# Performance work log

Hardware: AMD Instinct MI355X
Metric: run time of the kernel (lower is better)

The kernel has to match this reference:

```python
import jax, jax.numpy as jnp
import numpy as np

N_NODES = 50000
N_EDGES = 800000
IN_DIM, HID, OUT = 64, 128, 32
BN_EPS = 1e-5


def setup_inputs() -> dict:
    key = jax.random.key(0)
    ks = jax.random.split(key, 24)
    def w(k, shape, fan_in):
        return jax.random.normal(k, shape, dtype=jnp.float32) * (1.0 / np.sqrt(fan_in))
    inp = {
        "x": jax.random.normal(ks[0], (N_NODES, IN_DIM), dtype=jnp.float32),
        "edge_index": jax.random.randint(ks[1], (2, N_EDGES), 0, N_NODES, dtype=jnp.int64),
        # layer 0 GIN MLP: in -> hid -> hid
        "w1_0": w(ks[2], (IN_DIM, HID), IN_DIM), "b1_0": jnp.zeros((HID,), jnp.float32),
        "w2_0": w(ks[3], (HID, HID), HID),       "b2_0": jnp.zeros((HID,), jnp.float32),
        # skip projection for layer 0 (in_dim != hidden_dim -> Linear)
        "skip_w": w(ks[4], (IN_DIM, HID), IN_DIM), "skip_b": jnp.zeros((HID,), jnp.float32),
        # batchnorm params (layers 0 and 1 only)
        "bn_g0": jnp.ones((HID,), jnp.float32), "bn_b0": jnp.zeros((HID,), jnp.float32),
        # layer 1 GIN MLP: hid -> hid -> hid
        "w1_1": w(ks[5], (HID, HID), HID), "b1_1": jnp.zeros((HID,), jnp.float32),
        "w2_1": w(ks[6], (HID, HID), HID), "b2_1": jnp.zeros((HID,), jnp.float32),
        "bn_g1": jnp.ones((HID,), jnp.float32), "bn_b1": jnp.zeros((HID,), jnp.float32),
        # layer 2 GIN MLP: hid -> hid -> out
        "w1_2": w(ks[7], (HID, HID), HID), "b1_2": jnp.zeros((HID,), jnp.float32),
        "w2_2": w(ks[8], (HID, OUT), HID), "b2_2": jnp.zeros((OUT,), jnp.float32),
    }
    return inp


def _gin_conv(h, src, dst, n, W1, b1, W2, b2):
    # GINConv (eps=0): mlp((1+eps)*x_i + sum_{j in N(i)} x_j)
    agg = jax.ops.segment_sum(h[src], dst, num_segments=n)  # [N, d]
    z = h + agg
    return jax.nn.relu(z @ W1 + b1) @ W2 + b2


def _bn(h, g, b):
    # training-mode batchnorm over nodes (batch statistics, biased var)
    m = h.mean(0)
    v = jnp.mean((h - m) ** 2, axis=0)
    return g * (h - m) * jax.lax.rsqrt(v + BN_EPS) + b


def reference(x, edge_index, w1_0, b1_0, w2_0, b2_0, skip_w, skip_b, bn_g0, bn_b0,
              w1_1, b1_1, w2_1, b2_1, bn_g1, bn_b1, w1_2, b1_2, w2_2, b2_2):
    src, dst = edge_index[0], edge_index[1]
    n = x.shape[0]
    # layer 0: conv -> bn -> +skip_proj(residual) -> relu (dropout = identity in eval)
    h = _gin_conv(x, src, dst, n, w1_0, b1_0, w2_0, b2_0)
    h = _bn(h, bn_g0, bn_b0)
    h = h + (x @ skip_w + skip_b)
    residual = h
    h = jax.nn.relu(h)
    # layer 1: conv -> bn -> +residual (Identity skip) -> relu
    h = _gin_conv(h, src, dst, n, w1_1, b1_1, w2_1, b2_1)
    h = _bn(h, bn_g1, bn_b1)
    h = h + residual
    h = jax.nn.relu(h)
    # layer 2: conv only (no bn since i >= len(bns), no skip/relu since i == num_layers-1)
    h = _gin_conv(h, src, dst, n, w1_2, b1_2, w2_2, b2_2)
    return h
```

## Files before the change

kernel.cpp:

```cpp
#include <hip/hip_runtime.h>
#include <hip/hip_bf16.h>


#define HID 128
#define NPART 8
#define ABLK 256
#define BBLK 128
#define CAP 64

typedef __attribute__((ext_vector_type(8))) __bf16 bf16x8;
typedef __attribute__((ext_vector_type(4))) float f32x4;

__device__ __forceinline__ ushort f2b(float f) {
    uint u = __builtin_bit_cast(uint, f);
    u = (u + 0x7fffu + ((u >> 16) & 1u)) >> 16;
    return (ushort)u;
}
__device__ __forceinline__ float b2f(ushort s) {
    return __builtin_bit_cast(float, (uint)s << 16);
}
__device__ __forceinline__ float lo16(uint u) { return __builtin_bit_cast(float, u << 16); }
__device__ __forceinline__ float hi16(uint u) { return __builtin_bit_cast(float, u & 0xffff0000u); }
__device__ __forceinline__ uint packbf(float a, float b) {
    return (uint)f2b(a) | ((uint)f2b(b) << 16);
}

__launch_bounds__(256)
__global__ void ecount_kernel(const int* __restrict__ ei, int* __restrict__ bc,
                              int E, int pchunk) {
    __shared__ int cnt[NPART];
    if (threadIdx.x < NPART) cnt[threadIdx.x] = 0;
    __syncthreads();
    const int epb = (E + ABLK - 1) / ABLK;
    const int e0 = blockIdx.x * epb, e1 = min(e0 + epb, E);
    for (int e = e0 + threadIdx.x; e < e1; e += 256) {
        int d = ei[E + e];
        atomicAdd(&cnt[d / pchunk], 1);
    }
    __syncthreads();
    if (threadIdx.x < NPART) bc[threadIdx.x * ABLK + blockIdx.x] = cnt[threadIdx.x];
}

__launch_bounds__(1024)
__global__ void escan_kernel(int* __restrict__ bc) {
    __shared__ int ls[1024];
    const int t = threadIdx.x;
    const int v0 = bc[2 * t], v1 = bc[2 * t + 1];
    ls[t] = v0 + v1;
    __syncthreads();
    for (int off = 1; off < 1024; off <<= 1) {
        int tmp = (t >= off) ? ls[t - off] : 0;
        __syncthreads();
        ls[t] += tmp;
        __syncthreads();
    }
    const int excl = ls[t] - (v0 + v1);
    bc[2 * t] = excl;
    bc[2 * t + 1] = excl + v0;
}

__launch_bounds__(256)
__global__ void edist_kernel(const int* __restrict__ ei, const int* __restrict__ bc,
                             int2* __restrict__ ebuf, int E, int pchunk) {
    __shared__ int base[NPART];
    if (threadIdx.x < NPART) base[threadIdx.x] = bc[threadIdx.x * ABLK + blockIdx.x];
    __syncthreads();
    const int epb = (E + ABLK - 1) / ABLK;
    const int e0 = blockIdx.x * epb, e1 = min(e0 + epb, E);
    for (int e = e0 + threadIdx.x; e < e1; e += 256) {
        int s = ei[e], d = ei[E + e];
        int pos = atomicAdd(&base[d / pchunk], 1);
        ebuf[pos] = make_int2(s, d);
    }
}

__launch_bounds__(256)
__global__ void scatterf_kernel(const int2* __restrict__ ebuf, const int* __restrict__ bc,
                                int* __restrict__ deg, int* __restrict__ csr, int E) {
    const int part = blockIdx.x & (NPART - 1);
    const int blk  = blockIdx.x >> 3;
    const int pstart = bc[part * ABLK];
    const int pend = (part == NPART - 1) ? E : bc[(part + 1) * ABLK];
    const int epb = (pend - pstart + BBLK - 1) / BBLK;
    const int e0 = pstart + blk * epb, e1 = min(e0 + epb, pend);
    for (int e = e0 + threadIdx.x; e < e1; e += 256) {
        int2 ed = ebuf[e];
        int slot = atomicAdd(&deg[ed.y], 1);
        if (slot < CAP) csr[((size_t)ed.y << 6) + slot] = ed.x;
    }
}

__launch_bounds__(256)
__global__ void padfill_kernel(const int* __restrict__ deg, int* __restrict__ csr,
                               int* __restrict__ rowlen, int n) {
    const int nd = blockIdx.x * 256 + threadIdx.x;
    if (nd >= n) return;
    const int d = min(deg[nd], CAP);
    const int pd = min((d + 7) & ~7, CAP);
    for (int q = d; q < pd; q++) csr[((size_t)nd << 6) + q] = n;
    rowlen[nd] = pd;
}

struct PrepAll {
    const float* src[7];
    ushort* dst[7];
    int K[7];
    int N[7];
    int off[8];
};

__launch_bounds__(256)
__global__ void wprep_kernel(PrepAll a) {
    const int b = blockIdx.x;
    int m = 0;
    while (m < 6 && b >= a.off[m + 1]) m++;
    const int K = a.K[m], N = a.N[m];
    const int e = (b - a.off[m]) * 256 + threadIdx.x;
    if (e >= K * N) return;
    const int n = e / K, k = e % K;
    a.dst[m][e] = f2b(a.src[m][(size_t)k * N + n]);
}

__global__ void x2bf_kernel(const float* __restrict__ x, ushort* __restrict__ xb,
                            float* __restrict__ bn0, float* __restrict__ bn1,
                            int* __restrict__ deg, uint* __restrict__ xb_sent,
                            uint* __restrict__ agg_sent, int n, int total4) {
    const int gi = blockIdx.x * 256 + threadIdx.x;
    if (gi < 2048) { bn0[gi] = 0.f; bn1[gi] = 0.f; }
    if (blockIdx.x == 0) {
        if (threadIdx.x < 64) agg_sent[threadIdx.x] = 0;
        else if (threadIdx.x < 96) xb_sent[threadIdx.x - 64] = 0;
    }
    if (gi < n) deg[gi] = 0;
    if (gi < total4) {
        float4 v = reinterpret_cast<const float4*>(x)[gi];
        ushort4 o;
        o.x = f2b(v.x); o.y = f2b(v.y); o.z = f2b(v.z); o.w = f2b(v.w);
        reinterpret_cast<ushort4*>(xb)[gi] = o;
    }
}

template <int K1, int NC2, bool SKIP, bool OUTBF, bool STATS>
__launch_bounds__(512)
__global__ void fused_layer(const ushort* __restrict__ table,
                            const int* __restrict__ rowlen, const int* __restrict__ csr,
                            const ushort* __restrict__ W1t, const float* __restrict__ b1,
                            const ushort* __restrict__ W2t, const float* __restrict__ b2,
                            float* __restrict__ convf, ushort* __restrict__ convb,
                            const ushort* __restrict__ skw, const float* __restrict__ skb,
                            float* __restrict__ skipout, float* __restrict__ bnsums,
                            int M) {
    __shared__ ushort Zt[64 * K1];
    __shared__ ushort Yt[64 * 128];
    __shared__ float bnloc[STATS ? 256 : 1];
    const int tid = threadIdx.x;
    const int w = tid >> 6, lane = tid & 63;
    const int rb0 = blockIdx.x * 64;
    constexpr int ZROWB = K1 * 2;

    if (STATS && tid < 256) bnloc[tid] = 0.f;

    if constexpr (K1 == 128) {
        const uint* t2 = reinterpret_cast<const uint*>(table);
#pragma unroll
        for (int i = 0; i < 8; i++) {
            const int rt = w * 8 + i;
            const int nd = min(rb0 + rt, M - 1);
            const int s = nd << 6;
            const int e = s + rowlen[nd];
            uint v = t2[(size_t)nd * 64 + lane];
            float ax = lo16(v), ay = hi16(v);
            for (int k = s; k < e; k += 8) {
#pragma unroll
                for (int j = 0; j < 8; j++) {
                    uint u = t2[(size_t)csr[k + j] * 64 + lane];
                    ax += lo16(u);
                    ay += hi16(u);
                }
            }
            *reinterpret_cast<uint*>(reinterpret_cast<char*>(Zt) +
                (((uint)(rt * 256 + lane * 4)) ^ ((rt & 7) << 4))) = packbf(ax, ay);
        }
    } else {
        const uint* t2 = reinterpret_cast<const uint*>(table);
        const int half = lane >> 5, li = lane & 31;
#pragma unroll
        for (int i = 0; i < 4; i++) {
            const int rt = w * 8 + i * 2 + half;
            const int nd = min(rb0 + rt, M - 1);
            const int s = nd << 6;
            const int e = s + rowlen[nd];
            uint v = t2[(size_t)nd * 32 + li];
            float ax = lo16(v), ay = hi16(v);
            for (int k = s; k < e; k += 8) {
#pragma unroll
                for (int j = 0; j < 8; j++) {
                    uint u = t2[(size_t)csr[k + j] * 32 + li];
                    ax += lo16(u);
                    ay += hi16(u);
                }
            }
            *reinterpret_cast<uint*>(reinterpret_cast<char*>(Zt) +
                (((uint)(rt * 128 + li * 4)) ^ ((rt & 7) << 4))) = packbf(ax, ay);
        }
    }
    __syncthreads();

    const int wr = w >> 2, wc = w & 3;
    const int lr = lane & 15, hg = lane >> 4;
    const int xorv = (lr & 7) << 4;

    {
        f32x4 a00 = {}, a01 = {}, a10 = {}, a11 = {};
#pragma unroll
        for (int k0 = 0; k0 < K1; k0 += 32) {
            const uint o0 = (uint)((wr * 32 + lr) * ZROWB + k0 * 2 + hg * 16) ^ xorv;
            const uint o1 = (uint)((wr * 32 + 16 + lr) * ZROWB + k0 * 2 + hg * 16) ^ xorv;
            bf16x8 za0 = *reinterpret_cast<const bf16x8*>(reinterpret_cast<const char*>(Zt) + o0);
            bf16x8 za1 = *reinterpret_cast<const bf16x8*>(reinterpret_cast<const char*>(Zt) + o1);
            bf16x8 wb0 = *reinterpret_cast<const bf16x8*>(W1t + (size_t)(wc * 32 + lr) * K1 + k0 + hg * 8);
            bf16x8 wb1 = *reinterpret_cast<const bf16x8*>(W1t + (size_t)(wc * 32 + 16 + lr) * K1 + k0 + hg * 8);
            a00 = __builtin_amdgcn_mfma_f32_16x16x32_bf16(za0, wb0, a00, 0, 0, 0);
            a01 = __builtin_amdgcn_mfma_f32_16x16x32_bf16(za0, wb1, a01, 0, 0, 0);
            a10 = __builtin_amdgcn_mfma_f32_16x16x32_bf16(za1, wb0, a10, 0, 0, 0);
            a11 = __builtin_amdgcn_mfma_f32_16x16x32_bf16(za1, wb1, a11, 0, 0, 0);
        }
        const int c0 = wc * 32 + lr, c1 = wc * 32 + 16 + lr;
        const float bv0 = b1[c0], bv1 = b1[c1];
        f32x4 accs[2][2] = {{a00, a01}, {a10, a11}};
#pragma unroll
        for (int m = 0; m < 2; m++) {
#pragma unroll
            for (int j = 0; j < 4; j++) {
                const int row = wr * 32 + m * 16 + hg * 4 + j;
                const uint sw = (uint)((row & 7) << 4);
                *reinterpret_cast<ushort*>(reinterpret_cast<char*>(Yt) + ((uint)(row * 256 + c0 * 2) ^ sw)) =
                    f2b(fmaxf(accs[m][0][j] + bv0, 0.f));
                *reinterpret_cast<ushort*>(reinterpret_cast<char*>(Yt) + ((uint)(row * 256 + c1 * 2) ^ sw)) =
                    f2b(fmaxf(accs[m][1][j] + bv1, 0.f));
            }
        }
    }
    __syncthreads();

    if constexpr (SKIP) {
        const uint* x2 = reinterpret_cast<const uint*>(table);
#pragma unroll
        for (int pp = 0; pp < 4; pp++) {
            const int rt = pp * 16 + (tid >> 5);
            const int cu = tid & 31;
            const int nd = min(rb0 + rt, M - 1);
            uint v = x2[(size_t)nd * 32 + cu];
            const uint boff = (uint)(rt * 128 + cu * 4) ^ ((rt & 7) << 4);
            *reinterpret_cast<uint*>(reinterpret_cast<char*>(Zt) + boff) = v;
        }
    }

    if (NC2 == 128 || w < 2) {
        const int wr2 = (NC2 == 128) ? wr : w;
        const int cb2 = (NC2 == 128) ? wc * 32 : 0;
        f32x4 d00 = {}, d01 = {}, d10 = {}, d11 = {};
#pragma unroll
        for (int k0 = 0; k0 < 128; k0 += 32) {
            const uint o0 = (uint)((wr2 * 32 + lr) * 256 + k0 * 2 + hg * 16) ^ xorv;
            const uint o1 = (uint)((wr2 * 32 + 16 + lr) * 256 + k0 * 2 + hg * 16) ^ xorv;
            bf16x8 ya0 = *reinterpret_cast<const bf16x8*>(reinterpret_cast<const char*>(Yt) + o0);
            bf16x8 ya1 = *reinterpret_cast<const bf16x8*>(reinterpret_cast<const char*>(Yt) + o1);
            bf16x8 wb0 = *reinterpret_cast<const bf16x8*>(W2t + (size_t)(cb2 + lr) * 128 + k0 + hg * 8);
            bf16x8 wb1 = *reinterpret_cast<const bf16x8*>(W2t + (size_t)(cb2 + 16 + lr) * 128 + k0 + hg * 8);
            d00 = __builtin_amdgcn_mfma_f32_16x16x32_bf16(ya0, wb0, d00, 0, 0, 0);
            d01 = __builtin_amdgcn_mfma_f32_16x16x32_bf16(ya0, wb1, d01, 0, 0, 0);
            d10 = __builtin_amdgcn_mfma_f32_16x16x32_bf16(ya1, wb0, d10, 0, 0, 0);
            d11 = __builtin_amdgcn_mfma_f32_16x16x32_bf16(ya1, wb1, d11, 0, 0, 0);
        }
        const int c0 = cb2 + lr, c1 = cb2 + 16 + lr;
        const float bv0 = b2[c0], bv1 = b2[c1];
        f32x4 accs[2][2] = {{d00, d01}, {d10, d11}};
        float s0 = 0.f, q0 = 0.f, s1 = 0.f, q1 = 0.f;
#pragma unroll
        for (int m = 0; m < 2; m++) {
#pragma unroll
            for (int j = 0; j < 4; j++) {
                const int row = rb0 + wr2 * 32 + m * 16 + hg * 4 + j;
                if (row < M) {
                    const float v0 = accs[m][0][j] + bv0;
                    const float v1 = accs[m][1][j] + bv1;
                    if (STATS) {
                        s0 += v0; q0 += v0 * v0;
                        s1 += v1; q1 += v1 * v1;
                    }
                    if constexpr (OUTBF) {
                        convb[(size_t)row * NC2 + c0] = f2b(v0);
                        convb[(size_t)row * NC2 + c1] = f2b(v1);
                    } else {
                        convf[(size_t)row * NC2 + c0] = v0;
                        convf[(size_t)row * NC2 + c1] = v1;
                    }
                }
            }
        }
        if (STATS) {
            atomicAdd(&bnloc[c0], s0);
            atomicAdd(&bnloc[c1], s1);
            atomicAdd(&bnloc[128 + c0], q0);
            atomicAdd(&bnloc[128 + c1], q1);
        }
    }

    if constexpr (SKIP) {
        __syncthreads();
        f32x4 s00 = {}, s01 = {}, s10 = {}, s11 = {};
#pragma unroll
        for (int k0 = 0; k0 < 64; k0 += 32) {
            const uint o0 = (uint)((wr * 32 + lr) * 128 + k0 * 2 + hg * 16) ^ xorv;
            const uint o1 = (uint)((wr * 32 + 16 + lr) * 128 + k0 * 2 + hg * 16) ^ xorv;
            bf16x8 za0 = *reinterpret_cast<const bf16x8*>(reinterpret_cast<const char*>(Zt) + o0);
            bf16x8 za1 = *reinterpret_cast<const bf16x8*>(reinterpret_cast<const char*>(Zt) + o1);
            bf16x8 wb0 = *reinterpret_cast<const bf16x8*>(skw + (size_t)(wc * 32 + lr) * 64 + k0 + hg * 8);
            bf16x8 wb1 = *reinterpret_cast<const bf16x8*>(skw + (size_t)(wc * 32 + 16 + lr) * 64 + k0 + hg * 8);
            s00 = __builtin_amdgcn_mfma_f32_16x16x32_bf16(za0, wb0, s00, 0, 0, 0);
            s01 = __builtin_amdgcn_mfma_f32_16x16x32_bf16(za0, wb1, s01, 0, 0, 0);
            s10 = __builtin_amdgcn_mfma_f32_16x16x32_bf16(za1, wb0, s10, 0, 0, 0);
            s11 = __builtin_amdgcn_mfma_f32_16x16x32_bf16(za1, wb1, s11, 0, 0, 0);
        }
        const int c0 = wc * 32 + lr, c1 = wc * 32 + 16 + lr;
        const float bv0 = skb[c0], bv1 = skb[c1];
        f32x4 accs[2][2] = {{s00, s01}, {s10, s11}};
#pragma unroll
        for (int m = 0; m < 2; m++) {
#pragma unroll
            for (int j = 0; j < 4; j++) {
                const int row = rb0 + wr * 32 + m * 16 + hg * 4 + j;
                if (row < M) {
                    skipout[(size_t)row * 128 + c0] = accs[m][0][j] + bv0;
                    skipout[(size_t)row * 128 + c1] = accs[m][1][j] + bv1;
                }
            }
        }
    }

    if constexpr (STATS) {
        __syncthreads();
        if (tid < 256) atomicAdd(&bnsums[((blockIdx.x & 7) << 8) + tid], bnloc[tid]);
    }
}

template <bool WRITE_RES>
__global__ void bn_apply_kernel(const ushort* __restrict__ conv, const float* __restrict__ sums,
                                const float* __restrict__ gamma, const float* __restrict__ beta,
                                const float* __restrict__ add, float* __restrict__ resf,
                                ushort* __restrict__ outb, int total2, int n) {
    int i = blockIdx.x * blockDim.x + threadIdx.x;
    if (i >= total2) return;
    const int c0 = (i & 63) * 2, c1 = c0 + 1;
    float S0 = 0.f, S1 = 0.f, Q0 = 0.f, Q1 = 0.f;
#pragma unroll
    for (int b = 0; b < 8; b++) {
        const float* bp = sums + (b << 8);
        S0 += bp[c0]; S1 += bp[c1];
        Q0 += bp[128 + c0]; Q1 += bp[128 + c1];
    }
    const float inv = 1.f / (float)n;
    const float m0 = S0 * inv, m1 = S1 * inv;
    const float v0 = Q0 * inv - m0 * m0;
    const float v1 = Q1 * inv - m1 * m1;
    const float sc0 = gamma[c0] * rsqrtf(v0 + 1e-5f);
    const float sc1 = gamma[c1] * rsqrtf(v1 + 1e-5f);
    const uint u = reinterpret_cast<const uint*>(conv)[i];
    const float2 ad = reinterpret_cast<const float2*>(add)[i];
    const float val0 = (lo16(u) - m0) * sc0 + beta[c0] + ad.x;
    const float val1 = (hi16(u) - m1) * sc1 + beta[c1] + ad.y;
    if (WRITE_RES) reinterpret_cast<float2*>(resf)[i] = make_float2(val0, val1);
    reinterpret_cast<uint*>(outb)[i] = packbf(fmaxf(val0, 0.f), fmaxf(val1, 0.f));
}

extern "C" void kernel_launch(void* const* d_in, const int* in_sizes, int n_in,
                              void* d_out, int out_size, void* d_ws, size_t ws_size,
                              hipStream_t stream) {
    const float* x      = (const float*)d_in[0];
    const int*   ei     = (const int*)d_in[1];
    const float* w1_0   = (const float*)d_in[2];
    const float* b1_0   = (const float*)d_in[3];
    const float* w2_0   = (const float*)d_in[4];
    const float* b2_0   = (const float*)d_in[5];
    const float* skip_w = (const float*)d_in[6];
    const float* skip_b = (const float*)d_in[7];
    const float* bn_g0  = (const float*)d_in[8];
    const float* bn_b0  = (const float*)d_in[9];
    const float* w1_1   = (const float*)d_in[10];
    const float* b1_1   = (const float*)d_in[11];
    const float* w2_1   = (const float*)d_in[12];
    const float* b2_1   = (const float*)d_in[13];
    const float* bn_g1  = (const float*)d_in[14];
    const float* bn_b1  = (const float*)d_in[15];
    const float* w1_2   = (const float*)d_in[16];
    const float* b1_2   = (const float*)d_in[17];
    const float* w2_2   = (const float*)d_in[18];
    const float* b2_2   = (const float*)d_in[19];

    const int N = in_sizes[0] / 64;
    const int E = in_sizes[1] / 2;
    const int pchunk = (N + NPART - 1) / NPART;

    char* p = (char*)d_ws;
    auto carve = [&](size_t bytes) -> void* {
        void* q = (void*)p;
        p += (bytes + 255) & ~(size_t)255;
        return q;
    };
    int*   deg    = (int*)carve((size_t)N * 4);
    int*   rowlen = (int*)carve((size_t)N * 4);
    int*   csr    = (int*)carve((size_t)N * CAP * 4);
    int*   bc     = (int*)carve((size_t)NPART * ABLK * 4);
    int2*  ebuf   = (int2*)carve((size_t)E * 8);
    float* bnsums0 = (float*)carve(2048 * 4);
    float* bnsums1 = (float*)carve(2048 * 4);
    ushort* w1_0t = (ushort*)carve(64 * 128 * 2);
    ushort* w2_0t = (ushort*)carve(128 * 128 * 2);
    ushort* skwt  = (ushort*)carve(64 * 128 * 2);
    ushort* w1_1t = (ushort*)carve(128 * 128 * 2);
    ushort* w2_1t = (ushort*)carve(128 * 128 * 2);
    ushort* w1_2t = (ushort*)carve(128 * 128 * 2);
    ushort* w2_2t = (ushort*)carve(128 * 32 * 2);
    ushort* x_bf  = (ushort*)carve((size_t)(N + 1) * 64 * 2);
    ushort* aggin = (ushort*)carve((size_t)(N + 1) * HID * 2);
    ushort* convB = (ushort*)carve((size_t)N * HID * 2);
    float* bufC_f = (float*)carve((size_t)N * HID * 4);

    const int NB  = (N + 255) / 256;
    const int EWB2 = (N * 64 + 255) / 256;
    const int FUSE_G = (N + 63) / 64;

    PrepAll pa;
    pa.src[0] = w1_0; pa.dst[0] = w1_0t; pa.K[0] = 64;  pa.N[0] = 128;
    pa.src[1] = w2_0; pa.dst[1] = w2_0t; pa.K[1] = 128; pa.N[1] = 128;
    pa.src[2] = skip_w; pa.dst[2] = skwt; pa.K[2] = 64; pa.N[2] = 128;
    pa.src[3] = w1_1; pa.dst[3] = w1_1t; pa.K[3] = 128; pa.N[3] = 128;
    pa.src[4] = w2_1; pa.dst[4] = w2_1t; pa.K[4] = 128; pa.N[4] = 128;
    pa.src[5] = w1_2; pa.dst[5] = w1_2t; pa.K[5] = 128; pa.N[5] = 128;
    pa.src[6] = w2_2; pa.dst[6] = w2_2t; pa.K[6] = 128; pa.N[6] = 32;
    int off = 0;
    for (int m = 0; m < 7; m++) { pa.off[m] = off; off += (pa.K[m] * pa.N[m]) / 256; }
    pa.off[7] = off;
    wprep_kernel<<<off, 256, 0, stream>>>(pa);
    x2bf_kernel<<<(N * 64 / 4 + 255) / 256, 256, 0, stream>>>(
        x, x_bf, bnsums0, bnsums1, deg,
        reinterpret_cast<uint*>(x_bf + (size_t)N * 64),
        reinterpret_cast<uint*>(aggin + (size_t)N * HID), N, N * 64 / 4);

    ecount_kernel<<<ABLK, 256, 0, stream>>>(ei, bc, E, pchunk);
    escan_kernel<<<1, 1024, 0, stream>>>(bc);
    edist_kernel<<<ABLK, 256, 0, stream>>>(ei, bc, ebuf, E, pchunk);
    scatterf_kernel<<<NPART * BBLK, 256, 0, stream>>>(ebuf, bc, deg, csr, E);
    padfill_kernel<<<NB, 256, 0, stream>>>(deg, csr, rowlen, N);

    fused_layer<64, 128, true, true, true><<<FUSE_G, 512, 0, stream>>>(
        x_bf, rowlen, csr, w1_0t, b1_0, w2_0t, b2_0, nullptr, convB, skwt, skip_b, bufC_f, bnsums0, N);
    bn_apply_kernel<true><<<EWB2, 256, 0, stream>>>(convB, bnsums0, bn_g0, bn_b0, bufC_f, bufC_f, aggin, N * 64, N);

    fused_layer<128, 128, false, true, true><<<FUSE_G, 512, 0, stream>>>(
        aggin, rowlen, csr, w1_1t, b1_1, w2_1t, b2_1, nullptr, convB, nullptr, nullptr, nullptr, bnsums1, N);
    bn_apply_kernel<false><<<EWB2, 256, 0, stream>>>(convB, bnsums1, bn_g1, bn_b1, bufC_f, nullptr, aggin, N * 64, N);

    fused_layer<128, 32, false, false, false><<<FUSE_G, 512, 0, stream>>>(
        aggin, rowlen, csr, w1_2t, b1_2, w2_2t, b2_2, (float*)d_out, nullptr, nullptr, nullptr, nullptr, nullptr, N);
}
```

Baseline: 266.9 us.

## Split aggregation into XCD-sliced gather kernel and separate MFMA MLP kernel

After: 394.7 us. 1.48x slower.

```diff
diff --git a/kernel.cpp b/kernel.cpp
--- a/kernel.cpp
+++ b/kernel.cpp
@@ -15,9 +15,6 @@
     uint u = __builtin_bit_cast(uint, f);
     u = (u + 0x7fffu + ((u >> 16) & 1u)) >> 16;
     return (ushort)u;
-}
-__device__ __forceinline__ float b2f(ushort s) {
-    return __builtin_bit_cast(float, (uint)s << 16);
 }
 __device__ __forceinline__ float lo16(uint u) { return __builtin_bit_cast(float, u << 16); }
 __device__ __forceinline__ float hi16(uint u) { return __builtin_bit_cast(float, u & 0xffff0000u); }
@@ -76,7 +73,7 @@
 
 __launch_bounds__(256)
 __global__ void scatterf_kernel(const int2* __restrict__ ebuf, const int* __restrict__ bc,
-                                int* __restrict__ deg, int* __restrict__ csr, int E) {
+                                int* __restrict__ deg, ushort* __restrict__ csr, int E) {
     const int part = blockIdx.x & (NPART - 1);
     const int blk  = blockIdx.x >> 3;
     const int pstart = bc[part * ABLK];
@@ -86,18 +83,18 @@
     for (int e = e0 + threadIdx.x; e < e1; e += 256) {
         int2 ed = ebuf[e];
         int slot = atomicAdd(&deg[ed.y], 1);
-        if (slot < CAP) csr[((size_t)ed.y << 6) + slot] = ed.x;
-    }
-}
-
-__launch_bounds__(256)
-__global__ void padfill_kernel(const int* __restrict__ deg, int* __restrict__ csr,
+        if (slot < CAP) csr[((size_t)ed.y << 6) + slot] = (ushort)ed.x;
+    }
+}
+
+__launch_bounds__(256)
+__global__ void padfill_kernel(const int* __restrict__ deg, ushort* __restrict__ csr,
                                int* __restrict__ rowlen, int n) {
     const int nd = blockIdx.x * 256 + threadIdx.x;
     if (nd >= n) return;
     const int d = min(deg[nd], CAP);
     const int pd = min((d + 7) & ~7, CAP);
-    for (int q = d; q < pd; q++) csr[((size_t)nd << 6) + q] = n;
+    for (int q = d; q < pd; q++) csr[((size_t)nd << 6) + q] = (ushort)n;
     rowlen[nd] = pd;
 }
 
@@ -140,99 +137,86 @@
     }
 }
 
+template <int RU, int NSLICE>
+__launch_bounds__(256)
+__global__ void agg_slice2(const ushort* __restrict__ table, const int* __restrict__ rowlen,
+                           const ushort* __restrict__ csr, ushort* __restrict__ z, int n) {
+    constexpr int NPARTN = 8 / NSLICE;
+    const int p8 = blockIdx.x & 7;
+    const int slice = p8 % NSLICE;
+    const int part = p8 / NSLICE;
+    const int cb = blockIdx.x >> 3;
+    const int npp = (n + NPARTN - 1) / NPARTN;
+    const int n0 = part * npp;
+    const int n1 = min(n0 + npp, n);
+    const int w = threadIdx.x >> 6, lane = threadIdx.x & 63;
+    const int li = lane & 15, qi = lane >> 4;
+    const int col = slice * 16 + li;
+    const uint* t2 = reinterpret_cast<const uint*>(table);
+    uint* z2 = reinterpret_cast<uint*>(z);
+    const int base = n0 + (cb * 4 + w) * 16;
+    for (int i = 0; i < 16; i++) {
+        const int nd = base + i;
+        if (nd >= n1) break;
+        const int s = nd << 6;
+        const int len = rowlen[nd];
+        uint sv = (qi == 0) ? t2[(size_t)nd * RU + col] : 0u;
+        float ax = lo16(sv), ay = hi16(sv);
+        for (int k = qi; k < len; k += 8) {
+            const int i0 = csr[s + k];
+            const int i1 = csr[s + k + 4];
+            const uint u0 = t2[(size_t)i0 * RU + col];
+            const uint u1 = t2[(size_t)i1 * RU + col];
+            ax += lo16(u0); ay += hi16(u0);
+            ax += lo16(u1); ay += hi16(u1);
+        }
+        ax += __shfl_xor(ax, 16); ay += __shfl_xor(ay, 16);
+        ax += __shfl_xor(ax, 32); ay += __shfl_xor(ay, 32);
+        if (qi == 0) z2[(size_t)nd * RU + col] = packbf(ax, ay);
+    }
+}
+
 template <int K1, int NC2, bool SKIP, bool OUTBF, bool STATS>
-__launch_bounds__(512)
-__global__ void fused_layer(const ushort* __restrict__ table,
-                            const int* __restrict__ rowlen, const int* __restrict__ csr,
-                            const ushort* __restrict__ W1t, const float* __restrict__ b1,
-                            const ushort* __restrict__ W2t, const float* __restrict__ b2,
-                            float* __restrict__ convf, ushort* __restrict__ convb,
-                            const ushort* __restrict__ skw, const float* __restrict__ skb,
-                            float* __restrict__ skipout, float* __restrict__ bnsums,
-                            int M) {
-    __shared__ ushort Zt[64 * K1];
-    __shared__ ushort Yt[64 * 128];
+__launch_bounds__(256)
+__global__ void mlp_layer(const ushort* __restrict__ Z,
+                          const ushort* __restrict__ W1t, const float* __restrict__ b1,
+                          const ushort* __restrict__ W2t, const float* __restrict__ b2,
+                          float* __restrict__ convf, ushort* __restrict__ convb,
+                          const ushort* __restrict__ skw, const float* __restrict__ skb,
+                          float* __restrict__ skipout, const ushort* __restrict__ xbf,
+                          float* __restrict__ bnsums, int M) {
+    __shared__ ushort Yt[32 * 128];
     __shared__ float bnloc[STATS ? 256 : 1];
     const int tid = threadIdx.x;
     const int w = tid >> 6, lane = tid & 63;
-    const int rb0 = blockIdx.x * 64;
-    constexpr int ZROWB = K1 * 2;
-
-    if (STATS && tid < 256) bnloc[tid] = 0.f;
-
-    if constexpr (K1 == 128) {
-        const uint* t2 = reinterpret_cast<const uint*>(table);
-#pragma unroll
-        for (int i = 0; i < 8; i++) {
-            const int rt = w * 8 + i;
-            const int nd = min(rb0 + rt, M - 1);
-            const int s = nd << 6;
-            const int e = s + rowlen[nd];
-            uint v = t2[(size_t)nd * 64 + lane];
-            float ax = lo16(v), ay = hi16(v);
-            for (int k = s; k < e; k += 8) {
-#pragma unroll
-                for (int j = 0; j < 8; j++) {
-                    uint u = t2[(size_t)csr[k + j] * 64 + lane];
-                    ax += lo16(u);
-                    ay += hi16(u);
-                }
-            }
-            *reinterpret_cast<uint*>(reinterpret_cast<char*>(Zt) +
-                (((uint)(rt * 256 + lane * 4)) ^ ((rt & 7) << 4))) = packbf(ax, ay);
-        }
-    } else {
-        const uint* t2 = reinterpret_cast<const uint*>(table);
-        const int half = lane >> 5, li = lane & 31;
-#pragma unroll
-        for (int i = 0; i < 4; i++) {
-            const int rt = w * 8 + i * 2 + half;
-            const int nd = min(rb0 + rt, M - 1);
-            const int s = nd << 6;
-            const int e = s + rowlen[nd];
-            uint v = t2[(size_t)nd * 32 + li];
-            float ax = lo16(v), ay = hi16(v);
-            for (int k = s; k < e; k += 8) {
-#pragma unroll
-                for (int j = 0; j < 8; j++) {
-                    uint u = t2[(size_t)csr[k + j] * 32 + li];
-                    ax += lo16(u);
-                    ay += hi16(u);
-                }
-            }
-            *reinterpret_cast<uint*>(reinterpret_cast<char*>(Zt) +
-                (((uint)(rt * 128 + li * 4)) ^ ((rt & 7) << 4))) = packbf(ax, ay);
-        }
-    }
-    __syncthreads();
-
-    const int wr = w >> 2, wc = w & 3;
+    const int rb0 = blockIdx.x * 32;
     const int lr = lane & 15, hg = lane >> 4;
     const int xorv = (lr & 7) << 4;
+    const int r0 = min(rb0 + lr, M - 1), r1 = min(rb0 + 16 + lr, M - 1);
+
+    if (STATS && tid < 256) bnloc[tid] = 0.f;
 
     {
         f32x4 a00 = {}, a01 = {}, a10 = {}, a11 = {};
 #pragma unroll
         for (int k0 = 0; k0 < K1; k0 += 32) {
-            const uint o0 = (uint)((wr * 32 + lr) * ZROWB + k0 * 2 + hg * 16) ^ xorv;
-            const uint o1 = (uint)((wr * 32 + 16 + lr) * ZROWB + k0 * 2 + hg * 16) ^ xorv;
-            bf16x8 za0 = *reinterpret_cast<const bf16x8*>(reinterpret_cast<const char*>(Zt) + o0);
-            bf16x8 za1 = *reinterpret_cast<const bf16x8*>(reinterpret_cast<const char*>(Zt) + o1);
-            bf16x8 wb0 = *reinterpret_cast<const bf16x8*>(W1t + (size_t)(wc * 32 + lr) * K1 + k0 + hg * 8);
-            bf16x8 wb1 = *reinterpret_cast<const bf16x8*>(W1t + (size_t)(wc * 32 + 16 + lr) * K1 + k0 + hg * 8);
+            bf16x8 za0 = *reinterpret_cast<const bf16x8*>(Z + (size_t)r0 * K1 + k0 + hg * 8);
+            bf16x8 za1 = *reinterpret_cast<const bf16x8*>(Z + (size_t)r1 * K1 + k0 + hg * 8);
+            bf16x8 wb0 = *reinterpret_cast<const bf16x8*>(W1t + (size_t)(w * 32 + lr) * K1 + k0 + hg * 8);
+            bf16x8 wb1 = *reinterpret_cast<const bf16x8*>(W1t + (size_t)(w * 32 + 16 + lr) * K1 + k0 + hg * 8);
             a00 = __builtin_amdgcn_mfma_f32_16x16x32_bf16(za0, wb0, a00, 0, 0, 0);
             a01 = __builtin_amdgcn_mfma_f32_16x16x32_bf16(za0, wb1, a01, 0, 0, 0);
             a10 = __builtin_amdgcn_mfma_f32_16x16x32_bf16(za1, wb0, a10, 0, 0, 0);
             a11 = __builtin_amdgcn_mfma_f32_16x16x32_bf16(za1, wb1, a11, 0, 0, 0);
         }
-        const int c0 = wc * 32 + lr, c1 = wc * 32 + 16 + lr;
+        const int c0 = w * 32 + lr, c1 = w * 32 + 16 + lr;
         const float bv0 = b1[c0], bv1 = b1[c1];
         f32x4 accs[2][2] = {{a00, a01}, {a10, a11}};
 #pragma unroll
         for (int m = 0; m < 2; m++) {
 #pragma unroll
             for (int j = 0; j < 4; j++) {
-                const int row = wr * 32 + m * 16 + hg * 4 + j;
+                const int row = m * 16 + hg * 4 + j;
                 const uint sw = (uint)((row & 7) << 4);
                 *reinterpret_cast<ushort*>(reinterpret_cast<char*>(Yt) + ((uint)(row * 256 + c0 * 2) ^ sw)) =
                     f2b(fmaxf(accs[m][0][j] + bv0, 0.f));
@@ -241,29 +225,44 @@
             }
         }
     }
+
+    if constexpr (SKIP) {
+        f32x4 s00 = {}, s01 = {}, s10 = {}, s11 = {};
+#pragma unroll
+        for (int k0 = 0; k0 < 64; k0 += 32) {
+            bf16x8 za0 = *reinterpret_cast<const bf16x8*>(xbf + (size_t)r0 * 64 + k0 + hg * 8);
+            bf16x8 za1 = *reinterpret_cast<const bf16x8*>(xbf + (size_t)r1 * 64 + k0 + hg * 8);
+            bf16x8 wb0 = *reinterpret_cast<const bf16x8*>(skw + (size_t)(w * 32 + lr) * 64 + k0 + hg * 8);
+            bf16x8 wb1 = *reinterpret_cast<const bf16x8*>(skw + (size_t)(w * 32 + 16 + lr) * 64 + k0 + hg * 8);
+            s00 = __builtin_amdgcn_mfma_f32_16x16x32_bf16(za0, wb0, s00, 0, 0, 0);
+            s01 = __builtin_amdgcn_mfma_f32_16x16x32_bf16(za0, wb1, s01, 0, 0, 0);
+            s10 = __builtin_amdgcn_mfma_f32_16x16x32_bf16(za1, wb0, s10, 0, 0, 0);
+            s11 = __builtin_amdgcn_mfma_f32_16x16x32_bf16(za1, wb1, s11, 0, 0, 0);
+        }
+        const int c0 = w * 32 + lr, c1 = w * 32 + 16 + lr;
+        const float bv0 = skb[c0], bv1 = skb[c1];
+        f32x4 accs[2][2] = {{s00, s01}, {s10, s11}};
+#pragma unroll
+        for (int m = 0; m < 2; m++) {
+#pragma unroll
+            for (int j = 0; j < 4; j++) {
+                const int row = rb0 + m * 16 + hg * 4 + j;
+                if (row < M) {
+                    skipout[(size_t)row * 128 + c0] = accs[m][0][j] + bv0;
+                    skipout[(size_t)row * 128 + c1] = accs[m][1][j] + bv1;
+                }
+            }
+        }
+    }
     __syncthreads();
 
-    if constexpr (SKIP) {
-        const uint* x2 = reinterpret_cast<const uint*>(table);
-#pragma unroll
-        for (int pp = 0; pp < 4; pp++) {
-            const int rt = pp * 16 + (tid >> 5);
-            const int cu = tid & 31;
-            const int nd = min(rb0 + rt, M - 1);
-            uint v = x2[(size_t)nd * 32 + cu];
-            const uint boff = (uint)(rt * 128 + cu * 4) ^ ((rt & 7) << 4);
-            *reinterpret_cast<uint*>(reinterpret_cast<char*>(Zt) + boff) = v;
-        }
-    }
-
-    if (NC2 == 128 || w < 2) {
-        const int wr2 = (NC2 == 128) ? wr : w;
-        const int cb2 = (NC2 == 128) ? wc * 32 : 0;
+    if (NC2 == 128 || w == 0) {
+        const int cb2 = (NC2 == 128) ? w * 32 : 0;
         f32x4 d00 = {}, d01 = {}, d10 = {}, d11 = {};
 #pragma unroll
         for (int k0 = 0; k0 < 128; k0 += 32) {
-            const uint o0 = (uint)((wr2 * 32 + lr) * 256 + k0 * 2 + hg * 16) ^ xorv;
-            const uint o1 = (uint)((wr2 * 32 + 16 + lr) * 256 + k0 * 2 + hg * 16) ^ xorv;
+            const uint o0 = (uint)(lr * 256 + k0 * 2 + hg * 16) ^ xorv;
+            const uint o1 = (uint)((16 + lr) * 256 + k0 * 2 + hg * 16) ^ xorv;
             bf16x8 ya0 = *reinterpret_cast<const bf16x8*>(reinterpret_cast<const char*>(Yt) + o0);
             bf16x8 ya1 = *reinterpret_cast<const bf16x8*>(reinterpret_cast<const char*>(Yt) + o1);
             bf16x8 wb0 = *reinterpret_cast<const bf16x8*>(W2t + (size_t)(cb2 + lr) * 128 + k0 + hg * 8);
@@ -281,7 +280,7 @@
         for (int m = 0; m < 2; m++) {
 #pragma unroll
             for (int j = 0; j < 4; j++) {
-                const int row = rb0 + wr2 * 32 + m * 16 + hg * 4 + j;
+                const int row = rb0 + m * 16 + hg * 4 + j;
                 if (row < M) {
                     const float v0 = accs[m][0][j] + bv0;
                     const float v1 = accs[m][1][j] + bv1;
@@ -304,38 +303,6 @@
             atomicAdd(&bnloc[c1], s1);
             atomicAdd(&bnloc[128 + c0], q0);
             atomicAdd(&bnloc[128 + c1], q1);
-        }
-    }
-
-    if constexpr (SKIP) {
-        __syncthreads();
-        f32x4 s00 = {}, s01 = {}, s10 = {}, s11 = {};
-#pragma unroll
-        for (int k0 = 0; k0 < 64; k0 += 32) {
-            const uint o0 = (uint)((wr * 32 + lr) * 128 + k0 * 2 + hg * 16) ^ xorv;
-            const uint o1 = (uint)((wr * 32 + 16 + lr) * 128 + k0 * 2 + hg * 16) ^ xorv;
-            bf16x8 za0 = *reinterpret_cast<const bf16x8*>(reinterpret_cast<const char*>(Zt) + o0);
-            bf16x8 za1 = *reinterpret_cast<const bf16x8*>(reinterpret_cast<const char*>(Zt) + o1);
-            bf16x8 wb0 = *reinterpret_cast<const bf16x8*>(skw + (size_t)(wc * 32 + lr) * 64 + k0 + hg * 8);
-            bf16x8 wb1 = *reinterpret_cast<const bf16x8*>(skw + (size_t)(wc * 32 + 16 + lr) * 64 + k0 + hg * 8);
-            s00 = __builtin_amdgcn_mfma_f32_16x16x32_bf16(za0, wb0, s00, 0, 0, 0);
-            s01 = __builtin_amdgcn_mfma_f32_16x16x32_bf16(za0, wb1, s01, 0, 0, 0);
-            s10 = __builtin_amdgcn_mfma_f32_16x16x32_bf16(za1, wb0, s10, 0, 0, 0);
-            s11 = __builtin_amdgcn_mfma_f32_16x16x32_bf16(za1, wb1, s11, 0, 0, 0);
-        }
-        const int c0 = wc * 32 + lr, c1 = wc * 32 + 16 + lr;
-        const float bv0 = skb[c0], bv1 = skb[c1];
-        f32x4 accs[2][2] = {{s00, s01}, {s10, s11}};
-#pragma unroll
-        for (int m = 0; m < 2; m++) {
-#pragma unroll
-            for (int j = 0; j < 4; j++) {
-                const int row = rb0 + wr * 32 + m * 16 + hg * 4 + j;
-                if (row < M) {
-                    skipout[(size_t)row * 128 + c0] = accs[m][0][j] + bv0;
-                    skipout[(size_t)row * 128 + c1] = accs[m][1][j] + bv1;
-                }
-            }
         }
     }
 
@@ -408,11 +375,11 @@
         p += (bytes + 255) & ~(size_t)255;
         return q;
     };
-    int*   deg    = (int*)carve((size_t)N * 4);
-    int*   rowlen = (int*)carve((size_t)N * 4);
-    int*   csr    = (int*)carve((size_t)N * CAP * 4);
-    int*   bc     = (int*)carve((size_t)NPART * ABLK * 4);
-    int2*  ebuf   = (int2*)carve((size_t)E * 8);
+    int*    deg    = (int*)carve((size_t)N * 4);
+    int*    rowlen = (int*)carve((size_t)N * 4);
+    ushort* csr    = (ushort*)carve((size_t)N * CAP * 2);
+    int*    bc     = (int*)carve((size_t)NPART * ABLK * 4);
+    int2*   ebuf   = (int2*)carve((size_t)E * 8);
     float* bnsums0 = (float*)carve(2048 * 4);
     float* bnsums1 = (float*)carve(2048 * 4);
     ushort* w1_0t = (ushort*)carve(64 * 128 * 2);
@@ -424,12 +391,17 @@
     ushort* w2_2t = (ushort*)carve(128 * 32 * 2);
     ushort* x_bf  = (ushort*)carve((size_t)(N + 1) * 64 * 2);
     ushort* aggin = (ushort*)carve((size_t)(N + 1) * HID * 2);
+    ushort* bufZ  = (ushort*)carve((size_t)N * HID * 2);
     ushort* convB = (ushort*)carve((size_t)N * HID * 2);
     float* bufC_f = (float*)carve((size_t)N * HID * 4);
 
     const int NB  = (N + 255) / 256;
     const int EWB2 = (N * 64 + 255) / 256;
-    const int FUSE_G = (N + 63) / 64;
+    const int MLP_G = (N + 31) / 32;
+    const int npp128 = (N + 1) / 2;
+    const int AGG128_G = 8 * ((npp128 + 63) / 64);
+    const int npp64 = (N + 3) / 4;
+    const int AGG64_G = 8 * ((npp64 + 63) / 64);
 
     PrepAll pa;
     pa.src[0] = w1_0; pa.dst[0] = w1_0t; pa.K[0] = 64;  pa.N[0] = 128;
@@ -454,14 +426,17 @@
     scatterf_kernel<<<NPART * BBLK, 256, 0, stream>>>(ebuf, bc, deg, csr, E);
     padfill_kernel<<<NB, 256, 0, stream>>>(deg, csr, rowlen, N);
 
-    fused_layer<64, 128, true, true, true><<<FUSE_G, 512, 0, stream>>>(
-        x_bf, rowlen, csr, w1_0t, b1_0, w2_0t, b2_0, nullptr, convB, skwt, skip_b, bufC_f, bnsums0, N);
+    agg_slice2<32, 2><<<AGG64_G, 256, 0, stream>>>(x_bf, rowlen, csr, bufZ, N);
+    mlp_layer<64, 128, true, true, true><<<MLP_G, 256, 0, stream>>>(
+        bufZ, w1_0t, b1_0, w2_0t, b2_0, nullptr, convB, skwt, skip_b, bufC_f, x_bf, bnsums0, N);
     bn_apply_kernel<true><<<EWB2, 256, 0, stream>>>(convB, bnsums0, bn_g0, bn_b0, bufC_f, bufC_f, aggin, N * 64, N);
 
-    fused_layer<128, 128, false, true, true><<<FUSE_G, 512, 0, stream>>>(
-        aggin, rowlen, csr, w1_1t, b1_1, w2_1t, b2_1, nullptr, convB, nullptr, nullptr, nullptr, bnsums1, N);
+    agg_slice2<64, 4><<<AGG128_G, 256, 0, stream>>>(aggin, rowlen, csr, bufZ, N);
+    mlp_layer<128, 128, false, true, true><<<MLP_G, 256, 0, stream>>>(
+        bufZ, w1_1t, b1_1, w2_1t, b2_1, nullptr, convB, nullptr, nullptr, nullptr, nullptr, bnsums1, N);
     bn_apply_kernel<false><<<EWB2, 256, 0, stream>>>(convB, bnsums1, bn_g1, bn_b1, bufC_f, nullptr, aggin, N * 64, N);
 
-    fused_layer<128, 32, false, false, false><<<FUSE_G, 512, 0, stream>>>(
-        aggin, rowlen, csr, w1_2t, b1_2, w2_2t, b2_2, (float*)d_out, nullptr, nullptr, nullptr, nullptr, nullptr, N);
-}
+    agg_slice2<64, 4><<<AGG128_G, 256, 0, stream>>>(aggin, rowlen, csr, bufZ, N);
+    mlp_layer<128, 32, false, false, false><<<MLP_G, 256, 0, stream>>>(
+        bufZ, w1_2t, b1_2, w2_2t, b2_2, (float*)d_out, nullptr, nullptr, nullptr, nullptr, nullptr, nullptr, N);
+}
```
